# Performance work log

Hardware: AMD Instinct MI355X
Metric: run time of the kernel (lower is better)

## Reference

```python
import jax, jax.numpy as jnp
import numpy as np

N, D, H, E = 50000, 512, 8, 3200000
DK = D // H  # 64


def setup_inputs() -> dict:
    key = jax.random.key(0)
    ks = jax.random.split(key, 12)
    x = jax.random.normal(ks[0], (N, D), dtype=jnp.float32)
    row_index = jnp.sort(jax.random.randint(ks[1], (E,), 0, N))
    col_index = jax.random.randint(ks[2], (E,), 0, N)
    att_bias = jax.random.normal(ks[3], (H, E), dtype=jnp.float32)
    # xavier-uniform-ish linear params (bias zero per module init)
    lim = np.sqrt(6.0 / (D + D)).astype(np.float32)
    def w(k):
        return jax.random.uniform(k, (D, D), minval=-lim, maxval=lim, dtype=jnp.float32)
    return {
        "x": x, "row_index": row_index, "col_index": col_index, "att_bias": att_bias,
        "Wq": w(ks[4]), "bq": jnp.zeros((D,), jnp.float32),
        "Wk": w(ks[5]), "bk": jnp.zeros((D,), jnp.float32),
        "Wv": w(ks[6]), "bv": jnp.zeros((D,), jnp.float32),
        "Wo": w(ks[7]), "bo": jnp.zeros((D,), jnp.float32),
    }


def _proj(x, W, b):
    # nn.Linear then reshape(N, H, DK).permute(1,0,2) -> [H, N, DK]
    return (x @ W.T + b).reshape(x.shape[0], H, DK).transpose(1, 0, 2)


def reference(x, row_index, col_index, att_bias, Wq, bq, Wk, bk, Wv, bv, Wo, bo):
    q = _proj(x, Wq, bq) / jnp.sqrt(jnp.float32(DK))  # [H,N,DK]
    k = _proj(x, Wk, bk)
    v = _proj(x, Wv, bv)
    n = x.shape[0]
    # masked QK^T at sparse (row,col) entries + additive sparse bias -> [H,E]
    logits = jnp.einsum("hed,hed->he", q[:, row_index], k[:, col_index]) + att_bias
    # per-row (segment) softmax over CSR rows, vmapped over heads
    seg_max = jax.vmap(lambda l: jax.ops.segment_max(l, row_index, num_segments=n))(logits)  # [H,N]
    p = jnp.exp(logits - seg_max[:, row_index])
    denom = jax.vmap(lambda pe: jax.ops.segment_sum(pe, row_index, num_segments=n))(p)  # [H,N]
    att = p / denom[:, row_index]  # [H,E]
    # sparse att @ V : scatter-add weighted value rows
    y = jax.vmap(lambda a, vc: jax.ops.segment_sum(a[:, None] * vc, row_index, num_segments=n))(
        att, v[:, col_index]
    )  # [H,N,DK]
    y = y.transpose(1, 0, 2).reshape(n, H * DK)  # [N,D]
    return y @ Wo.T + bo
```

## Files before the change

### kernel.cpp

```cpp
#include <hip/hip_runtime.h>
#include <hip/hip_bf16.h>
#include <cstddef>
#include <cstdint>


typedef __attribute__((ext_vector_type(8))) short bf16x8;
typedef __attribute__((ext_vector_type(4))) float f32x4;

#define KQ_SCALE 25.4f
#define KQ_DEQ   0.03937007874f

__device__ __forceinline__ void gload_lds16(const void* g, const void* l) {
    __builtin_amdgcn_global_load_lds(
        (const __attribute__((address_space(1))) unsigned int*)g,
        (__attribute__((address_space(3))) unsigned int*)l, 16, 0, 0);
}

__device__ __forceinline__ float bflo(unsigned u) { return __uint_as_float(u << 16); }
__device__ __forceinline__ float bfhi(unsigned u) { return __uint_as_float(u & 0xffff0000u); }
__device__ __forceinline__ float ub(unsigned u, int i) {
    return (float)((u >> (i * 8)) & 0xffu);
}

__device__ __forceinline__ void storeT(float* p, size_t i, float v) { p[i] = v; }
__device__ __forceinline__ void storeT(__hip_bfloat16* p, size_t i, float v) {
    p[i] = __float2bfloat16(v);
}
__device__ __forceinline__ void storeT(unsigned char* p, size_t i, float v) {
    const float q = fmaf(v, KQ_SCALE, 128.0f);
    p[i] = (unsigned char)__float2uint_rn(fminf(fmaxf(q, 0.f), 255.f));
}

__global__ __launch_bounds__(256) void conv_f32_bf16(
    const float* __restrict__ s, __hip_bfloat16* __restrict__ d, int n) {
    const int i = (blockIdx.x * 256 + threadIdx.x) * 8;
    if (i >= n) return;
    const float4 a = *(const float4*)(s + i);
    const float4 b = *(const float4*)(s + i + 4);
    alignas(16) __hip_bfloat16 o[8] = {
        __float2bfloat16(a.x), __float2bfloat16(a.y),
        __float2bfloat16(a.z), __float2bfloat16(a.w),
        __float2bfloat16(b.x), __float2bfloat16(b.y),
        __float2bfloat16(b.z), __float2bfloat16(b.w)};
    *(uint4*)(d + i) = *(const uint4*)o;
}

__global__ void row_start_kernel(const int* __restrict__ row_index,
                                 int* __restrict__ row_start, int n_rows, int E) {
    const int n = blockIdx.x * blockDim.x + threadIdx.x;
    if (n > n_rows) return;
    int lo = 0, hi = E;
    while (lo < hi) {
        const int mid = (lo + hi) >> 1;
        if (row_index[mid] < n) lo = mid + 1; else hi = mid;
    }
    row_start[n] = lo;
}

template <typename TO>
__global__ __launch_bounds__(256) void gemm_mfma_kernel(
    const short* __restrict__ A, const short* __restrict__ Bw,
    const float* __restrict__ bias, TO* __restrict__ C, int M, float scale) {
    __shared__ short As[2][128 * 32];
    __shared__ short Bs[2][128 * 32];
    const int t = threadIdx.x;
    const int w = t >> 6, l = t & 63;
    const int m0 = blockIdx.x * 128, n0 = blockIdx.y * 128;
    const int wrow = (w >> 1) * 64, wcol = (w & 1) * 64;
    const int fr = l & 15, fq = l >> 4;

    const int r0 = (w * 64 + l) >> 2, ko0 = ((w * 64 + l) & 3) * 8;
    int gmA0 = m0 + r0;      if (gmA0 >= M) gmA0 = M - 1;
    int gmA1 = m0 + r0 + 64; if (gmA1 >= M) gmA1 = M - 1;
    const int gnB0 = n0 + r0, gnB1 = n0 + r0 + 64;

    f32x4 acc[4][4];
#pragma unroll
    for (int mi = 0; mi < 4; ++mi)
#pragma unroll
        for (int ni = 0; ni < 4; ++ni) acc[mi][ni] = (f32x4){0.f, 0.f, 0.f, 0.f};

#define STAGE(buf, k0)                                                        \
    do {                                                                      \
        gload_lds16(A + (size_t)gmA0 * 512 + (k0) + ko0, &As[buf][w * 512]);  \
        gload_lds16(A + (size_t)gmA1 * 512 + (k0) + ko0, &As[buf][2048 + w * 512]); \
        gload_lds16(Bw + (size_t)gnB0 * 512 + (k0) + ko0, &Bs[buf][w * 512]); \
        gload_lds16(Bw + (size_t)gnB1 * 512 + (k0) + ko0, &Bs[buf][2048 + w * 512]); \
    } while (0)

    STAGE(0, 0);
    __syncthreads();

    for (int kt = 0; kt < 16; ++kt) {
        const int cur = kt & 1;
        if (kt + 1 < 16) STAGE(cur ^ 1, (kt + 1) * 32);

        bf16x8 af[4], bfr[4];
#pragma unroll
        for (int mi = 0; mi < 4; ++mi)
            af[mi] = *(const bf16x8*)(&As[cur][(wrow + mi * 16 + fr) * 32 + fq * 8]);
#pragma unroll
        for (int ni = 0; ni < 4; ++ni)
            bfr[ni] = *(const bf16x8*)(&Bs[cur][(wcol + ni * 16 + fr) * 32 + fq * 8]);
#pragma unroll
        for (int mi = 0; mi < 4; ++mi)
#pragma unroll
            for (int ni = 0; ni < 4; ++ni)
                acc[mi][ni] = __builtin_amdgcn_mfma_f32_16x16x32_bf16(
                    af[mi], bfr[ni], acc[mi][ni], 0, 0, 0);

        __syncthreads();
    }
#undef STAGE

#pragma unroll
    for (int mi = 0; mi < 4; ++mi)
#pragma unroll
        for (int ni = 0; ni < 4; ++ni)
#pragma unroll
            for (int r = 0; r < 4; ++r) {
                const int gr = m0 + wrow + mi * 16 + fq * 4 + r;
                if (gr < M) {
                    const int gc = n0 + wcol + ni * 16 + fr;
                    storeT(C, (size_t)gr * 512 + gc, (acc[mi][ni][r] + bias[gc]) * scale);
                }
            }
}

__global__ __launch_bounds__(256) void sparse_attn_kernel(
    const __hip_bfloat16* __restrict__ qb, const unsigned char* __restrict__ kq,
    const unsigned char* __restrict__ vq, const int* __restrict__ col_index,
    const float* __restrict__ att_bias, const int* __restrict__ row_start,
    __hip_bfloat16* __restrict__ yout, int E) {
    const int n = blockIdx.x;
    const int w = threadIdx.x >> 6;
    const int lane = threadIdx.x & 63;
    const int g = lane & 7;
    const int j = lane >> 3;
    const int hA = 2 * w + (g >> 2);
    const int dim0 = (g & 3) * 16;
    const int e0 = row_start[n], e1 = row_start[n + 1];

    const short* qp = (const short*)qb + (size_t)n * 512 + hA * 64 + dim0;
    float qf[16];
    {
        const uint4 a = *(const uint4*)qp;
        const uint4 b = *(const uint4*)(qp + 8);
        const unsigned* ua = (const unsigned*)&a;
        const unsigned* ubp = (const unsigned*)&b;
#pragma unroll
        for (int i = 0; i < 4; ++i) {
            qf[2 * i]     = bflo(ua[i]);
            qf[2 * i + 1] = bfhi(ua[i]);
            qf[8 + 2 * i]     = bflo(ubp[i]);
            qf[8 + 2 * i + 1] = bfhi(ubp[i]);
        }
    }
    float sumq = 0.f;
#pragma unroll
    for (int i = 0; i < 16; ++i) sumq += qf[i];
    sumq += __shfl_xor(sumq, 1, 64);
    sumq += __shfl_xor(sumq, 2, 64);
    const float qc = -128.0f * KQ_DEQ * sumq;

    const float* biasH = att_bias + (size_t)hA * (size_t)E;
    const unsigned pairoff = (unsigned)(w * 128 + g * 16);

    float acc[16];
#pragma unroll
    for (int i = 0; i < 16; ++i) acc[i] = 0.f;
    float s_lane = 0.f;

    if (e0 < e1) {
        const int e1m1 = e1 - 1;
        int ec = min(e0 + j, e1m1);
        unsigned co = ((unsigned)col_index[ec] << 9) + pairoff;
        uint4 ku = *(const uint4*)(kq + co);
        uint4 vu = *(const uint4*)(vq + co);
        float bv = __builtin_nontemporal_load(biasH + ec);
        bool vld = (e0 + j) < e1;

        for (int base = e0; base < e1; base += 8) {
            uint4 ku_n, vu_n; float bv_n = 0.f; bool vld_n = false;
            const int nbase = base + 8;
            if (nbase < e1) {
                const int ecn = min(nbase + j, e1m1);
                const unsigned con = ((unsigned)col_index[ecn] << 9) + pairoff;
                ku_n = *(const uint4*)(kq + con);
                vu_n = *(const uint4*)(vq + con);
                bv_n = __builtin_nontemporal_load(biasH + ecn);
                vld_n = (nbase + j) < e1;
            }

            float d = 0.f;
            {
                const unsigned* u = (const unsigned*)&ku;
#pragma unroll
                for (int i = 0; i < 4; ++i)
#pragma unroll
                    for (int b = 0; b < 4; ++b)
                        d = fmaf(qf[4 * i + b], ub(u[i], b), d);
            }
            d += __shfl_xor(d, 1, 64);
            d += __shfl_xor(d, 2, 64);
            const float lg = fmaf(KQ_DEQ, d, qc) + bv;
            const float p = vld ? __expf(lg) : 0.f;
            s_lane += p;
            {
                const unsigned* u = (const unsigned*)&vu;
#pragma unroll
                for (int i = 0; i < 4; ++i)
#pragma unroll
                    for (int b = 0; b < 4; ++b)
                        acc[4 * i + b] = fmaf(p, ub(u[i], b), acc[4 * i + b]);
            }

            ku = ku_n; vu = vu_n; bv = bv_n; vld = vld_n;
        }
    }

#pragma unroll
    for (int st = 8; st < 64; st <<= 1) s_lane += __shfl_xor(s_lane, st, 64);
#pragma unroll
    for (int i = 0; i < 16; ++i) {
#pragma unroll
        for (int st = 8; st < 64; st <<= 1) acc[i] += __shfl_xor(acc[i], st, 64);
    }

    float y0 = acc[0], y1 = acc[1];
#pragma unroll
    for (int t = 1; t < 8; ++t) {
        y0 = (j == t) ? acc[2 * t] : y0;
        y1 = (j == t) ? acc[2 * t + 1] : y1;
    }
    const size_t orow = (size_t)n * 512 + hA * 64 + dim0 + 2 * j;
    if (s_lane > 0.f) {
        const float inv = 1.0f / s_lane;
        yout[orow]     = __float2bfloat16(fmaf(KQ_DEQ, y0 * inv, -128.0f * KQ_DEQ));
        yout[orow + 1] = __float2bfloat16(fmaf(KQ_DEQ, y1 * inv, -128.0f * KQ_DEQ));
    } else {
        yout[orow]     = __float2bfloat16(0.f);
        yout[orow + 1] = __float2bfloat16(0.f);
    }
}

extern "C" void kernel_launch(void* const* d_in, const int* in_sizes, int n_in,
                              void* d_out, int out_size, void* d_ws, size_t ws_size,
                              hipStream_t stream) {
    const float* x         = (const float*)d_in[0];
    const int*   row_index = (const int*)d_in[1];
    const int*   col_index = (const int*)d_in[2];
    const float* att_bias  = (const float*)d_in[3];
    const float* Wq = (const float*)d_in[4];
    const float* bq = (const float*)d_in[5];
    const float* Wk = (const float*)d_in[6];
    const float* bk = (const float*)d_in[7];
    const float* Wv = (const float*)d_in[8];
    const float* bv = (const float*)d_in[9];
    const float* Wo = (const float*)d_in[10];
    const float* bo = (const float*)d_in[11];
    float* out = (float*)d_out;

    const int N = in_sizes[0] / 512;
    const int E = in_sizes[1];
    const int WN = 512 * 512;

    char* ws = (char*)d_ws;
    const size_t nb = (size_t)N * 512 * sizeof(__hip_bfloat16);
    const size_t b8 = (size_t)N * 512;
    const size_t wb = (size_t)WN * sizeof(__hip_bfloat16);
    __hip_bfloat16* xb  = (__hip_bfloat16*)(ws);
    __hip_bfloat16* qb  = (__hip_bfloat16*)(ws + nb);
    unsigned char*  kq8 = (unsigned char*)(ws + 2 * nb);
    unsigned char*  vq8 = (unsigned char*)(ws + 2 * nb + b8);
    __hip_bfloat16* wqb = (__hip_bfloat16*)(ws + 2 * nb + 2 * b8);
    __hip_bfloat16* wkb = (__hip_bfloat16*)(ws + 2 * nb + 2 * b8 + wb);
    __hip_bfloat16* wvb = (__hip_bfloat16*)(ws + 2 * nb + 2 * b8 + 2 * wb);
    __hip_bfloat16* wob = (__hip_bfloat16*)(ws + 2 * nb + 2 * b8 + 3 * wb);
    int* row_start = (int*)(ws + 2 * nb + 2 * b8 + 4 * wb);

    conv_f32_bf16<<<(N * 512 / 8 + 255) / 256, 256, 0, stream>>>(x, xb, N * 512);
    conv_f32_bf16<<<(WN / 8 + 255) / 256, 256, 0, stream>>>(Wq, wqb, WN);
    conv_f32_bf16<<<(WN / 8 + 255) / 256, 256, 0, stream>>>(Wk, wkb, WN);
    conv_f32_bf16<<<(WN / 8 + 255) / 256, 256, 0, stream>>>(Wv, wvb, WN);
    conv_f32_bf16<<<(WN / 8 + 255) / 256, 256, 0, stream>>>(Wo, wob, WN);

    row_start_kernel<<<(N + 1 + 255) / 256, 256, 0, stream>>>(row_index, row_start, N, E);

    const dim3 gg((N + 127) / 128, 4), gb(256);
    gemm_mfma_kernel<__hip_bfloat16><<<gg, gb, 0, stream>>>(
        (const short*)xb, (const short*)wqb, bq, qb, N, 0.125f);
    gemm_mfma_kernel<unsigned char><<<gg, gb, 0, stream>>>(
        (const short*)xb, (const short*)wkb, bk, kq8, N, 1.0f);
    gemm_mfma_kernel<unsigned char><<<gg, gb, 0, stream>>>(
        (const short*)xb, (const short*)wvb, bv, vq8, N, 1.0f);

    sparse_attn_kernel<<<N, 256, 0, stream>>>(
        qb, kq8, vq8, col_index, att_bias, row_start, xb , E);

    gemm_mfma_kernel<float><<<gg, gb, 0, stream>>>(
        (const short*)xb, (const short*)wob, bo, out, N, 1.0f);
}
```

Baseline: 834.3 us.

## Use single-buffered K=64 GEMM tiles and unroll sparse attention edge loop by two

The GEMM drops its double-buffered 32-wide K stages for a single-buffered 64-wide K tile, with a sync before and after each load. That halves the number of k-iterations and barriers but removes the overlap of loads with MFMA work. The sparse attention loop no longer prefetches the next group in software. It now processes two groups of 8 edges per iteration with independent loads, relying on memory-level parallelism from more outstanding gathers. The bias load also changes from nontemporal to a plain load.

```diff
diff --git a/kernel.cpp b/kernel.cpp
--- a/kernel.cpp
+++ b/kernel.cpp
@@ -61,18 +61,24 @@
 __global__ __launch_bounds__(256) void gemm_mfma_kernel(
     const short* __restrict__ A, const short* __restrict__ Bw,
     const float* __restrict__ bias, TO* __restrict__ C, int M, float scale) {
-    __shared__ short As[2][128 * 32];
-    __shared__ short Bs[2][128 * 32];
+    __shared__ short As[128 * 64];
+    __shared__ short Bs[128 * 64];
     const int t = threadIdx.x;
     const int w = t >> 6, l = t & 63;
     const int m0 = blockIdx.x * 128, n0 = blockIdx.y * 128;
     const int wrow = (w >> 1) * 64, wcol = (w & 1) * 64;
     const int fr = l & 15, fq = l >> 4;
 
-    const int r0 = (w * 64 + l) >> 2, ko0 = ((w * 64 + l) & 3) * 8;
-    int gmA0 = m0 + r0;      if (gmA0 >= M) gmA0 = M - 1;
-    int gmA1 = m0 + r0 + 64; if (gmA1 >= M) gmA1 = M - 1;
-    const int gnB0 = n0 + r0, gnB1 = n0 + r0 + 64;
+    const int r0 = (w * 64 + l) >> 3;
+    const int ko0 = ((w * 64 + l) & 7) * 8;
+    int gmA[4], gnB[4];
+#pragma unroll
+    for (int i = 0; i < 4; ++i) {
+        int gm = m0 + r0 + i * 32;
+        gmA[i] = (gm < M) ? gm : (M - 1);
+        gnB[i] = n0 + r0 + i * 32;
+    }
+    const int dstoff = (w * 64 + l) * 8;
 
     f32x4 acc[4][4];
 #pragma unroll
@@ -80,38 +86,32 @@
 #pragma unroll
         for (int ni = 0; ni < 4; ++ni) acc[mi][ni] = (f32x4){0.f, 0.f, 0.f, 0.f};
 
-#define STAGE(buf, k0)                                                        \
-    do {                                                                      \
-        gload_lds16(A + (size_t)gmA0 * 512 + (k0) + ko0, &As[buf][w * 512]);  \
-        gload_lds16(A + (size_t)gmA1 * 512 + (k0) + ko0, &As[buf][2048 + w * 512]); \
-        gload_lds16(Bw + (size_t)gnB0 * 512 + (k0) + ko0, &Bs[buf][w * 512]); \
-        gload_lds16(Bw + (size_t)gnB1 * 512 + (k0) + ko0, &Bs[buf][2048 + w * 512]); \
-    } while (0)
-
-    STAGE(0, 0);
-    __syncthreads();
-
-    for (int kt = 0; kt < 16; ++kt) {
-        const int cur = kt & 1;
-        if (kt + 1 < 16) STAGE(cur ^ 1, (kt + 1) * 32);
-
-        bf16x8 af[4], bfr[4];
-#pragma unroll
-        for (int mi = 0; mi < 4; ++mi)
-            af[mi] = *(const bf16x8*)(&As[cur][(wrow + mi * 16 + fr) * 32 + fq * 8]);
-#pragma unroll
-        for (int ni = 0; ni < 4; ++ni)
-            bfr[ni] = *(const bf16x8*)(&Bs[cur][(wcol + ni * 16 + fr) * 32 + fq * 8]);
-#pragma unroll
-        for (int mi = 0; mi < 4; ++mi)
+    for (int k0 = 0; k0 < 512; k0 += 64) {
+        __syncthreads();
+#pragma unroll
+        for (int i = 0; i < 4; ++i) {
+            gload_lds16(A + (size_t)gmA[i] * 512 + k0 + ko0, As + i * 2048 + dstoff);
+            gload_lds16(Bw + (size_t)gnB[i] * 512 + k0 + ko0, Bs + i * 2048 + dstoff);
+        }
+        __syncthreads();
+
+#pragma unroll
+        for (int kk = 0; kk < 2; ++kk) {
+            bf16x8 af[4], bfr[4];
+#pragma unroll
+            for (int mi = 0; mi < 4; ++mi)
+                af[mi] = *(const bf16x8*)(As + (wrow + mi * 16 + fr) * 64 + kk * 32 + fq * 8);
 #pragma unroll
             for (int ni = 0; ni < 4; ++ni)
-                acc[mi][ni] = __builtin_amdgcn_mfma_f32_16x16x32_bf16(
-                    af[mi], bfr[ni], acc[mi][ni], 0, 0, 0);
-
-        __syncthreads();
-    }
-#undef STAGE
+                bfr[ni] = *(const bf16x8*)(Bs + (wcol + ni * 16 + fr) * 64 + kk * 32 + fq * 8);
+#pragma unroll
+            for (int mi = 0; mi < 4; ++mi)
+#pragma unroll
+                for (int ni = 0; ni < 4; ++ni)
+                    acc[mi][ni] = __builtin_amdgcn_mfma_f32_16x16x32_bf16(
+                        af[mi], bfr[ni], acc[mi][ni], 0, 0, 0);
+        }
+    }
 
 #pragma unroll
     for (int mi = 0; mi < 4; ++mi)
@@ -173,49 +173,52 @@
 
     if (e0 < e1) {
         const int e1m1 = e1 - 1;
-        int ec = min(e0 + j, e1m1);
-        unsigned co = ((unsigned)col_index[ec] << 9) + pairoff;
-        uint4 ku = *(const uint4*)(kq + co);
-        uint4 vu = *(const uint4*)(vq + co);
-        float bv = __builtin_nontemporal_load(biasH + ec);
-        bool vld = (e0 + j) < e1;
-
-        for (int base = e0; base < e1; base += 8) {
-            uint4 ku_n, vu_n; float bv_n = 0.f; bool vld_n = false;
-            const int nbase = base + 8;
-            if (nbase < e1) {
-                const int ecn = min(nbase + j, e1m1);
-                const unsigned con = ((unsigned)col_index[ecn] << 9) + pairoff;
-                ku_n = *(const uint4*)(kq + con);
-                vu_n = *(const uint4*)(vq + con);
-                bv_n = __builtin_nontemporal_load(biasH + ecn);
-                vld_n = (nbase + j) < e1;
+        for (int base = e0; base < e1; base += 16) {
+            const int eA = base + j, eB = base + 8 + j;
+            const int ecA = min(eA, e1m1), ecB = min(eB, e1m1);
+            const int cA = col_index[ecA], cB = col_index[ecB];
+            const unsigned coA = ((unsigned)cA << 9) + pairoff;
+            const unsigned coB = ((unsigned)cB << 9) + pairoff;
+            const uint4 kuA = *(const uint4*)(kq + coA);
+            const uint4 vuA = *(const uint4*)(vq + coA);
+            const uint4 kuB = *(const uint4*)(kq + coB);
+            const uint4 vuB = *(const uint4*)(vq + coB);
+            const float bvA = biasH[ecA];
+            const float bvB = biasH[ecB];
+
+            float dA = 0.f, dB = 0.f;
+            {
+                const unsigned* uA = (const unsigned*)&kuA;
+                const unsigned* uB = (const unsigned*)&kuB;
+#pragma unroll
+                for (int i = 0; i < 4; ++i)
+#pragma unroll
+                    for (int b = 0; b < 4; ++b) {
+                        dA = fmaf(qf[4 * i + b], ub(uA[i], b), dA);
+                        dB = fmaf(qf[4 * i + b], ub(uB[i], b), dB);
+                    }
             }
-
-            float d = 0.f;
+            dA += __shfl_xor(dA, 1, 64);
+            dB += __shfl_xor(dB, 1, 64);
+            dA += __shfl_xor(dA, 2, 64);
+            dB += __shfl_xor(dB, 2, 64);
+            const float lgA = fmaf(KQ_DEQ, dA, qc) + bvA;
+            const float lgB = fmaf(KQ_DEQ, dB, qc) + bvB;
+            const float pA = (eA < e1) ? __expf(lgA) : 0.f;
+            const float pB = (eB < e1) ? __expf(lgB) : 0.f;
+            s_lane += pA + pB;
+
             {
-                const unsigned* u = (const unsigned*)&ku;
+                const unsigned* uA = (const unsigned*)&vuA;
+                const unsigned* uB = (const unsigned*)&vuB;
 #pragma unroll
                 for (int i = 0; i < 4; ++i)
 #pragma unroll
-                    for (int b = 0; b < 4; ++b)
-                        d = fmaf(qf[4 * i + b], ub(u[i], b), d);
+                    for (int b = 0; b < 4; ++b) {
+                        acc[4 * i + b] = fmaf(pA, ub(uA[i], b), acc[4 * i + b]);
+                        acc[4 * i + b] = fmaf(pB, ub(uB[i], b), acc[4 * i + b]);
+                    }
             }
-            d += __shfl_xor(d, 1, 64);
-            d += __shfl_xor(d, 2, 64);
-            const float lg = fmaf(KQ_DEQ, d, qc) + bv;
-            const float p = vld ? __expf(lg) : 0.f;
-            s_lane += p;
-            {
-                const unsigned* u = (const unsigned*)&vu;
-#pragma unroll
-                for (int i = 0; i < 4; ++i)
-#pragma unroll
-                    for (int b = 0; b < 4; ++b)
-                        acc[4 * i + b] = fmaf(p, ub(u[i], b), acc[4 * i + b]);
-            }
-
-            ku = ku_n; vu = vu_n; bv = bv_n; vld = vld_n;
         }
     }
 
```

New measurement: 827.4 us. Within noise of the previous version (-0.8%).
